# Kernel tuning notes

Hardware: AMD Instinct MI355X
Metric: run time of the kernel (lower is better)

Reference implementation:

```python
import jax, jax.numpy as jnp
import numpy as np

N = 100000   # nodes
E = 1600000  # edges
D = 128      # input feature dim
H = 64       # hidden dim
G = 64       # graphs in batch


def setup_inputs() -> dict:
    key = jax.random.key(0)
    ks = jax.random.split(key, 12)
    x = jax.random.normal(ks[0], (N, D), dtype=jnp.float32)
    ei = jax.random.randint(ks[1], (2, E), 0, N, dtype=jnp.int32)
    ew = jax.random.uniform(ks[2], (E,), dtype=jnp.float32)
    b = jnp.sort(jax.random.randint(ks[3], (N,), 0, G, dtype=jnp.int32))
    s = 0.05
    W1 = jax.random.normal(ks[4], (D, H), jnp.float32) * s
    b1 = jnp.zeros((H,), jnp.float32)
    W2 = jax.random.normal(ks[5], (H, H), jnp.float32) * s
    b2 = jnp.zeros((H,), jnp.float32)
    Wm1 = jax.random.normal(ks[6], (H, 32), jnp.float32) * s
    bm1 = jnp.zeros((32,), jnp.float32)
    Wm2 = jax.random.normal(ks[7], (32, 1), jnp.float32) * s
    bm2 = jnp.zeros((1,), jnp.float32)
    return {"x": x, "ei": ei, "ew": ew, "b": b,
            "W1": W1, "b1": b1, "W2": W2, "b2": b2,
            "Wm1": Wm1, "bm1": bm1, "Wm2": Wm2, "bm2": bm2}


def _gcn_norm(ei, ew, n):
    # PyG gcn_norm with add_self_loops=True (self-loop weight 1)
    loops = jnp.arange(n, dtype=ei.dtype)
    row = jnp.concatenate([ei[0], loops])
    col = jnp.concatenate([ei[1], loops])
    w = jnp.concatenate([ew, jnp.ones((n,), ew.dtype)])
    deg = jax.ops.segment_sum(w, col, num_segments=n)
    dinv = jnp.where(deg > 0, jax.lax.rsqrt(deg), 0.0)
    norm = dinv[row] * w * dinv[col]  # [E+N]
    return row, col, norm


def _gcn_conv(x, W, bias, row, col, norm, n):
    h = x @ W                                   # [N,H] small GEMM
    msg = h[row] * norm[:, None]                # gather over edges
    return jax.ops.segment_sum(msg, col, num_segments=n) + bias


def reference(x, ei, ew, b, W1, b1, W2, b2, Wm1, bm1, Wm2, bm2):
    n = x.shape[0]
    row, col, norm = _gcn_norm(ei, ew, n)
    h = jax.nn.relu(_gcn_conv(x, W1, b1, row, col, norm, n))
    h = jax.nn.relu(_gcn_conv(h, W2, b2, row, col, norm, n))
    # global_mean_pool over batch vector b
    sums = jax.ops.segment_sum(h, b, num_segments=G)
    cnt = jax.ops.segment_sum(jnp.ones((n,), h.dtype), b, num_segments=G)
    pooled = sums / jnp.maximum(cnt, 1.0)[:, None]  # [G,H]
    # MLP head: Linear(H,32) -> ReLU -> Linear(32,1)
    return jax.nn.relu(pooled @ Wm1 + bm1) @ Wm2 + bm2
```

## Files before the change

### kernel.cpp

```cpp
#include <hip/hip_runtime.h>
#include <hip/hip_bf16.h>
#include <hip/hip_fp16.h>


#define DIMH 64
#define BSH 7
#define BSZ 128
#define NBUCK_MAX 1024
#define EPB 4096
#define ESTRIDE 3072
#define CSTRIDE 4096

typedef _Float16 v8h __attribute__((ext_vector_type(8)));
typedef float v4f __attribute__((ext_vector_type(4)));

__global__ __launch_bounds__(512) void k_part(const int* __restrict__ row,
                                              const int* __restrict__ col,
                                              const float* __restrict__ ew,
                                              int* __restrict__ cursor,
                                              unsigned long long* __restrict__ part,
                                              int E, int nbuck) {
    __shared__ int h[NBUCK_MAX];
    __shared__ int h2[NBUCK_MAX];
    __shared__ int st[NBUCK_MAX];
    for (int i = threadIdx.x; i < nbuck; i += 512) { h[i] = 0; h2[i] = 0; }
    __syncthreads();
    int ebeg = blockIdx.x * EPB;
    int eend = min(ebeg + EPB, E);
    for (int e = ebeg + threadIdx.x; e < eend; e += 512)
        atomicAdd(&h[col[e] >> BSH], 1);
    __syncthreads();
    for (int i = threadIdx.x; i < nbuck; i += 512) {
        int c = h[i];
        st[i] = c ? i * ESTRIDE + atomicAdd(&cursor[i], c) : 0;
    }
    __syncthreads();
    for (int e = ebeg + threadIdx.x; e < eend; e += 512) {
        int c = col[e];
        int b = c >> BSH;
        int r = atomicAdd(&h2[b], 1);
        int slot = st[b] + r;
        if (slot < (b + 1) * ESTRIDE) {
            unsigned long long rec =
                ((unsigned long long)__float_as_uint(ew[e]) << 32) |
                ((unsigned long long)(unsigned)row[e] << 8) |
                (unsigned)(c & (BSZ - 1));
            part[slot] = rec;
        }
    }
}

__global__ __launch_bounds__(256) void k_sortB(const unsigned long long* __restrict__ part,
                                               const int* __restrict__ cursor,
                                               int2* __restrict__ csr,
                                               unsigned* __restrict__ rp,
                                               float* __restrict__ dinv, int N) {
    __shared__ int cnt[BSZ];
    __shared__ int scn[BSZ];
    __shared__ int cur[BSZ];
    __shared__ float dg[BSZ];
    int b = blockIdx.x;
    int nb0 = b << BSH;
    int nn = min(BSZ, N - nb0);
    int tid = threadIdx.x;
    if (tid < BSZ) { cnt[tid] = 0; dg[tid] = 1.0f; }
    __syncthreads();
    int ebeg = b * ESTRIDE;
    int eend = ebeg + min(cursor[b], ESTRIDE);
    for (int e = ebeg + tid; e < eend; e += 256)
        atomicAdd(&cnt[(int)(part[e] & (BSZ - 1))], 1);
    __syncthreads();
    int pc = 0;
    if (tid < BSZ) pc = min((cnt[tid] + 7) & ~7, 504);
    if (tid < BSZ) scn[tid] = pc;
    __syncthreads();
    for (int o = 1; o < BSZ; o <<= 1) {
        int t = 0;
        if (tid >= o && tid < BSZ) t = scn[tid - o];
        __syncthreads();
        if (tid >= o && tid < BSZ) scn[tid] += t;
        __syncthreads();
    }
    int Pb = b * CSTRIDE;
    int pofs = 0;
    if (tid < BSZ) {
        pofs = scn[tid] - pc;
        cur[tid] = pofs;
        if (tid < nn)
            rp[nb0 + tid] = ((unsigned)(pc >> 3) << 26) | (unsigned)(Pb + pofs);
    }
    __syncthreads();
    for (int e = ebeg + tid; e < eend; e += 256) {
        unsigned long long rec = part[e];
        int cl = (int)(rec & (BSZ - 1));
        float w = __uint_as_float((unsigned)(rec >> 32));
        int slot = atomicAdd(&cur[cl], 1);
        csr[Pb + slot] = make_int2((int)((rec >> 8) & 0xFFFFFF), __float_as_int(w));
        atomicAdd(&dg[cl], w);
    }
    __syncthreads();
    if (tid < nn) {
        int c = min(cnt[tid], pc);
        for (int k = c; k < pc; k++)
            csr[Pb + pofs + k] = make_int2(nb0 + tid, 0);
        dinv[nb0 + tid] = rsqrtf(dg[tid]);
    }
}

__global__ __launch_bounds__(256) void k_gemm_mfma(const float* __restrict__ X,
                                                   const float* __restrict__ W,
                                                   const float* __restrict__ dinv,
                                                   __half* __restrict__ Y, int n) {
    __shared__ _Float16 Wh[128 * 64];
    int tid = threadIdx.x;
    for (int i = tid * 4; i < 128 * 64; i += 256 * 4) {
        float4 w = *(const float4*)&W[i];
        Wh[i]     = (_Float16)w.x;
        Wh[i + 1] = (_Float16)w.y;
        Wh[i + 2] = (_Float16)w.z;
        Wh[i + 3] = (_Float16)w.w;
    }
    __syncthreads();

    int wv = tid >> 6;
    int lane = tid & 63;
    int m = lane & 15;
    int quad = lane >> 4;
    int tile = blockIdx.x * 4 + wv;
    int ntiles = (n + 15) >> 4;
    if (tile >= ntiles) return;

    v8h bf[4][4];
#pragma unroll
    for (int nt = 0; nt < 4; nt++)
#pragma unroll
        for (int s = 0; s < 4; s++)
#pragma unroll
            for (int j = 0; j < 8; j++)
                bf[nt][s][j] = Wh[(s * 32 + quad * 8 + j) * 64 + nt * 16 + m];

    v4f acc[4];
#pragma unroll
    for (int nt = 0; nt < 4; nt++) acc[nt] = (v4f){0.f, 0.f, 0.f, 0.f};

    int row = min(tile * 16 + m, n - 1);
    const float* xr = X + (size_t)row * 128;
#pragma unroll
    for (int s = 0; s < 4; s++) {
        float4 lo = *(const float4*)&xr[s * 32 + quad * 8];
        float4 hi = *(const float4*)&xr[s * 32 + quad * 8 + 4];
        v8h af;
        af[0] = (_Float16)lo.x; af[1] = (_Float16)lo.y;
        af[2] = (_Float16)lo.z; af[3] = (_Float16)lo.w;
        af[4] = (_Float16)hi.x; af[5] = (_Float16)hi.y;
        af[6] = (_Float16)hi.z; af[7] = (_Float16)hi.w;
#pragma unroll
        for (int nt = 0; nt < 4; nt++)
            acc[nt] = __builtin_amdgcn_mfma_f32_16x16x32_f16(af, bf[nt][s], acc[nt], 0, 0, 0);
    }

#pragma unroll
    for (int r = 0; r < 4; r++) {
        int node = tile * 16 + quad * 4 + r;
        if (node < n) {
            float di = dinv[node];
#pragma unroll
            for (int nt = 0; nt < 4; nt++)
                Y[(size_t)node * DIMH + nt * 16 + m] = __float2half(di * acc[nt][r]);
        }
    }
}

__global__ __launch_bounds__(256) void k_agg1f(const __half* __restrict__ Hin,
                                               const unsigned* __restrict__ rp,
                                               const int2* __restrict__ csr,
                                               const float* __restrict__ dinv,
                                               const float* __restrict__ bias,
                                               const float* __restrict__ W2,
                                               __half* __restrict__ T2, int n) {
    __shared__ float W2s[DIMH * DIMH];
    __shared__ unsigned hbuf[4][32];
    int tid = threadIdx.x;
    for (int i = tid * 4; i < DIMH * DIMH; i += 256 * 4)
        *(float4*)&W2s[i] = *(const float4*)&W2[i];
    __syncthreads();

    int lane = tid & 63;
    int wv = tid >> 6;
    int fp = lane & 31;
    bool hi = lane >= 32;
    const unsigned* HinU = (const unsigned*)Hin;
    int ngroups = (n + 3) >> 2;

    for (int grp = blockIdx.x; grp < ngroups; grp += gridDim.x) {
        int node = grp * 4 + wv;
        if (node >= n) continue;
        unsigned pk = rp[node];
        int p = (int)(pk & 0x3FFFFFFu);
        int iters = (int)(pk >> 26);
        float ax = 0.f, ay = 0.f;
        if (!hi) {
            unsigned su = HinU[(size_t)node * 32 + fp];
            float2 sf = __half22float2(*(__half2*)&su);
            ax = sf.x; ay = sf.y;
        }
        for (int it = 0; it < iters; it++, p += 8) {
            int4 m0 = *(const int4*)&csr[p];
            int4 m1 = *(const int4*)&csr[p + 2];
            int4 m2 = *(const int4*)&csr[p + 4];
            int4 m3 = *(const int4*)&csr[p + 6];
            int   s0 = hi ? m0.z : m0.x;
            float w0 = __int_as_float(hi ? m0.w : m0.y);
            int   s1 = hi ? m1.z : m1.x;
            float w1 = __int_as_float(hi ? m1.w : m1.y);
            int   s2 = hi ? m2.z : m2.x;
            float w2 = __int_as_float(hi ? m2.w : m2.y);
            int   s3 = hi ? m3.z : m3.x;
            float w3 = __int_as_float(hi ? m3.w : m3.y);
            unsigned u0 = HinU[(size_t)s0 * 32 + fp];
            unsigned u1 = HinU[(size_t)s1 * 32 + fp];
            unsigned u2 = HinU[(size_t)s2 * 32 + fp];
            unsigned u3 = HinU[(size_t)s3 * 32 + fp];
            float2 f0 = __half22float2(*(__half2*)&u0);
            float2 f1 = __half22float2(*(__half2*)&u1);
            float2 f2 = __half22float2(*(__half2*)&u2);
            float2 f3 = __half22float2(*(__half2*)&u3);
            ax += w0 * f0.x; ay += w0 * f0.y;
            ax += w1 * f1.x; ay += w1 * f1.y;
            ax += w2 * f2.x; ay += w2 * f2.y;
            ax += w3 * f3.x; ay += w3 * f3.y;
        }
        ax += __shfl_xor(ax, 32, 64);
        ay += __shfl_xor(ay, 32, 64);
        float di = dinv[node];
        if (!hi) {
            float vx = di * ax + bias[2 * fp];
            float vy = di * ay + bias[2 * fp + 1];
            vx = vx > 0.f ? vx : 0.f;
            vy = vy > 0.f ? vy : 0.f;
            __half2 hh = __floats2half2_rn(vx, vy);
            hbuf[wv][fp] = *(unsigned*)&hh;
        }
        float acc2 = 0.f;
        const unsigned* hb = hbuf[wv];
#pragma unroll
        for (int k8 = 0; k8 < 8; k8++) {
            uint4 hc = *(const uint4*)&hb[k8 * 4];
            float2 g0 = __half22float2(*(__half2*)&hc.x);
            float2 g1 = __half22float2(*(__half2*)&hc.y);
            float2 g2 = __half22float2(*(__half2*)&hc.z);
            float2 g3 = __half22float2(*(__half2*)&hc.w);
            const float* wc = &W2s[(k8 * 8) * DIMH + lane];
            acc2 += g0.x * wc[0 * DIMH] + g0.y * wc[1 * DIMH]
                  + g1.x * wc[2 * DIMH] + g1.y * wc[3 * DIMH]
                  + g2.x * wc[4 * DIMH] + g2.y * wc[5 * DIMH]
                  + g3.x * wc[6 * DIMH] + g3.y * wc[7 * DIMH];
        }
        T2[(size_t)node * DIMH + lane] = __float2half(di * acc2);
    }
}

__global__ __launch_bounds__(256) void k_aggN(const __half* __restrict__ Hin,
                                              const unsigned* __restrict__ rp,
                                              const int2* __restrict__ csr,
                                              const float* __restrict__ dinv,
                                              const float* __restrict__ bias,
                                              __half* __restrict__ Hout, int n) {
    int lane = threadIdx.x & 63;
    int wv = threadIdx.x >> 6;
    int node = blockIdx.x * 4 + wv;
    if (node >= n) return;
    unsigned pk = rp[node];
    int p = (int)(pk & 0x3FFFFFFu);
    int iters = (int)(pk >> 26);
    int fp = lane & 31;
    bool hi = lane >= 32;
    const unsigned* HinU = (const unsigned*)Hin;
    float ax = 0.f, ay = 0.f;
    if (!hi) {
        unsigned su = HinU[(size_t)node * 32 + fp];
        float2 sf = __half22float2(*(__half2*)&su);
        ax = sf.x; ay = sf.y;
    }
    for (int it = 0; it < iters; it++, p += 8) {
        int4 m0 = *(const int4*)&csr[p];
        int4 m1 = *(const int4*)&csr[p + 2];
        int4 m2 = *(const int4*)&csr[p + 4];
        int4 m3 = *(const int4*)&csr[p + 6];
        int   s0 = hi ? m0.z : m0.x;
        float w0 = __int_as_float(hi ? m0.w : m0.y);
        int   s1 = hi ? m1.z : m1.x;
        float w1 = __int_as_float(hi ? m1.w : m1.y);
        int   s2 = hi ? m2.z : m2.x;
        float w2 = __int_as_float(hi ? m2.w : m2.y);
        int   s3 = hi ? m3.z : m3.x;
        float w3 = __int_as_float(hi ? m3.w : m3.y);
        unsigned u0 = HinU[(size_t)s0 * 32 + fp];
        unsigned u1 = HinU[(size_t)s1 * 32 + fp];
        unsigned u2 = HinU[(size_t)s2 * 32 + fp];
        unsigned u3 = HinU[(size_t)s3 * 32 + fp];
        float2 f0 = __half22float2(*(__half2*)&u0);
        float2 f1 = __half22float2(*(__half2*)&u1);
        float2 f2 = __half22float2(*(__half2*)&u2);
        float2 f3 = __half22float2(*(__half2*)&u3);
        ax += w0 * f0.x; ay += w0 * f0.y;
        ax += w1 * f1.x; ay += w1 * f1.y;
        ax += w2 * f2.x; ay += w2 * f2.y;
        ax += w3 * f3.x; ay += w3 * f3.y;
    }
    ax += __shfl_xor(ax, 32, 64);
    ay += __shfl_xor(ay, 32, 64);
    if (!hi) {
        float di = dinv[node];
        float vx = di * ax + bias[2 * fp];
        float vy = di * ay + bias[2 * fp + 1];
        vx = vx > 0.f ? vx : 0.f;
        vy = vy > 0.f ? vy : 0.f;
        __half2 o = __floats2half2_rn(vx, vy);
        *(__half2*)&Hout[(size_t)node * DIMH + 2 * fp] = o;
    }
}

__global__ __launch_bounds__(256) void k_pool(const __half* __restrict__ Hin,
                                              const int* __restrict__ b,
                                              float* __restrict__ sums,
                                              float* __restrict__ cntG, int n) {
    const int CHUNK = 64;
    int lane = threadIdx.x & 63;
    int wave = threadIdx.x >> 6;
    int start = (blockIdx.x * 4 + wave) * CHUNK;
    if (start >= n) return;
    int end = min(start + CHUNK, n);
    float acc = 0.f;
    int g_cur = b[start];
    int cnt_local = 0;
    for (int i = start; i < end; i++) {
        int g = b[i];
        if (g != g_cur) {
            atomicAdd(&sums[g_cur * DIMH + lane], acc);
            if (lane == 0) atomicAdd(&cntG[g_cur], (float)cnt_local);
            acc = 0.f;
            cnt_local = 0;
            g_cur = g;
        }
        acc += __half2float(Hin[(size_t)i * DIMH + lane]);
        cnt_local++;
    }
    atomicAdd(&sums[g_cur * DIMH + lane], acc);
    if (lane == 0) atomicAdd(&cntG[g_cur], (float)cnt_local);
}

__global__ __launch_bounds__(64) void k_mlp(const float* __restrict__ sums,
                                            const float* __restrict__ cntG,
                                            const float* __restrict__ Wm1,
                                            const float* __restrict__ bm1,
                                            const float* __restrict__ Wm2,
                                            const float* __restrict__ bm2,
                                            float* __restrict__ out, int G) {
    int g = threadIdx.x;
    if (g >= G) return;
    float c = cntG[g];
    float inv = 1.f / (c > 1.f ? c : 1.f);
    float pooled[DIMH];
#pragma unroll
    for (int k = 0; k < DIMH; k++) pooled[k] = sums[g * DIMH + k] * inv;
    float o = 0.f;
    for (int j = 0; j < 32; j++) {
        float t = bm1[j];
#pragma unroll
        for (int k = 0; k < DIMH; k++) t += pooled[k] * Wm1[k * 32 + j];
        t = t > 0.f ? t : 0.f;
        o += t * Wm2[j];
    }
    out[g] = o + bm2[0];
}


extern "C" void kernel_launch(void* const* d_in, const int* in_sizes, int n_in,
                              void* d_out, int out_size, void* d_ws, size_t ws_size,
                              hipStream_t stream) {
    const float* x   = (const float*)d_in[0];
    const int*   ei  = (const int*)d_in[1];
    const float* ew  = (const float*)d_in[2];
    const int*   bvec= (const int*)d_in[3];
    const float* W1  = (const float*)d_in[4];
    const float* b1  = (const float*)d_in[5];
    const float* W2  = (const float*)d_in[6];
    const float* b2  = (const float*)d_in[7];
    const float* Wm1 = (const float*)d_in[8];
    const float* bm1 = (const float*)d_in[9];
    const float* Wm2 = (const float*)d_in[10];
    const float* bm2 = (const float*)d_in[11];
    float* out = (float*)d_out;

    const int E = in_sizes[2];
    const int N = in_sizes[3];
    const int G = out_size;
    const int* row = ei;
    const int* col = ei + E;
    const int nbuck = (N + BSZ - 1) >> BSH;

    char* p = (char*)d_ws;
    auto alloc = [&](size_t bytes) {
        void* r = (void*)p;
        p += (bytes + 255) & ~(size_t)255;
        return r;
    };

    unsigned long long* part = (unsigned long long*)alloc((size_t)nbuck * ESTRIDE * 8);
    int2*  csr    = (int2*)alloc((size_t)nbuck * CSTRIDE * 8);
    unsigned* rp  = (unsigned*)alloc((size_t)N * 4);
    float* dinv   = (float*)alloc((size_t)N * 4);
    __half* hA    = (__half*)alloc((size_t)N * DIMH * 2);
    __half* hB    = (__half*)alloc((size_t)N * DIMH * 2);
    int zeroInts  = nbuck + G * DIMH + G;
    int* cursor   = (int*)alloc((size_t)zeroInts * 4);
    float* sums   = (float*)(cursor + nbuck);
    float* cntG   = sums + G * DIMH;

    hipMemsetAsync(cursor, 0, (size_t)zeroInts * 4, stream);

    const int PB = (E + EPB - 1) / EPB;
    const int NT = (N + 15) / 16;

    k_part<<<PB, 512, 0, stream>>>(row, col, ew, cursor, part, E, nbuck);
    k_sortB<<<nbuck, 256, 0, stream>>>(part, cursor, csr, rp, dinv, N);

    k_gemm_mfma<<<(NT + 3) / 4, 256, 0, stream>>>(x, W1, dinv, hA, N);

    k_agg1f<<<4096, 256, 0, stream>>>(hA, rp, csr, dinv, b1, W2, hB, N);

    k_aggN<<<(N + 3) / 4, 256, 0, stream>>>(hB, rp, csr, dinv, b2, hA, N);

    k_pool<<<(N + 255) / 256, 256, 0, stream>>>(hA, bvec, sums, cntG, N);
    k_mlp<<<1, 64, 0, stream>>>(sums, cntG, Wm1, bm1, Wm2, bm2, out, G);
}
```

Baseline: 336.2 us.

## Split wave into four edge quarters with 8-byte gathers and MFMA layer-2 transform

The aggregation kernels now split each wave into four 16-lane groups, each gathering one 4-half (8-byte) feature slice per neighbor. Each iteration covers 16 edges instead of 8, so CSR padding moves to multiples of 16. The fused layer-1 kernel replaces its scalar LDS matvec with W2 in fp16 LDS and MFMA 16x16x32 instructions, keeping the B fragments in registers. This aims to raise the number of gathers in flight per wave and cut ALU work, at the cost of more padding edges, extra shuffle reductions and fp16 rounding of W2.

```diff
diff --git a/kernel.cpp b/kernel.cpp
--- a/kernel.cpp
+++ b/kernel.cpp
@@ -71,7 +71,7 @@
         atomicAdd(&cnt[(int)(part[e] & (BSZ - 1))], 1);
     __syncthreads();
     int pc = 0;
-    if (tid < BSZ) pc = min((cnt[tid] + 7) & ~7, 504);
+    if (tid < BSZ) pc = min((cnt[tid] + 15) & ~15, 496);
     if (tid < BSZ) scn[tid] = pc;
     __syncthreads();
     for (int o = 1; o < BSZ; o <<= 1) {
@@ -87,7 +87,7 @@
         pofs = scn[tid] - pc;
         cur[tid] = pofs;
         if (tid < nn)
-            rp[nb0 + tid] = ((unsigned)(pc >> 3) << 26) | (unsigned)(Pb + pofs);
+            rp[nb0 + tid] = ((unsigned)(pc >> 4) << 26) | (unsigned)(Pb + pofs);
     }
     __syncthreads();
     for (int e = ebeg + tid; e < eend; e += 256) {
@@ -178,85 +178,96 @@
                                                const float* __restrict__ bias,
                                                const float* __restrict__ W2,
                                                __half* __restrict__ T2, int n) {
-    __shared__ float W2s[DIMH * DIMH];
-    __shared__ unsigned hbuf[4][32];
+    __shared__ _Float16 W2h[DIMH * DIMH];
+    __shared__ __align__(16) _Float16 hbuf[4][DIMH];
     int tid = threadIdx.x;
-    for (int i = tid * 4; i < DIMH * DIMH; i += 256 * 4)
-        *(float4*)&W2s[i] = *(const float4*)&W2[i];
+    for (int i = tid * 4; i < DIMH * DIMH; i += 256 * 4) {
+        float4 w = *(const float4*)&W2[i];
+        W2h[i]     = (_Float16)w.x;
+        W2h[i + 1] = (_Float16)w.y;
+        W2h[i + 2] = (_Float16)w.z;
+        W2h[i + 3] = (_Float16)w.w;
+    }
     __syncthreads();
 
     int lane = tid & 63;
     int wv = tid >> 6;
-    int fp = lane & 31;
-    bool hi = lane >= 32;
-    const unsigned* HinU = (const unsigned*)Hin;
+    int q = lane >> 4;
+    int fp = lane & 15;
+
+    v8h bf[4][2];
+#pragma unroll
+    for (int nt = 0; nt < 4; nt++)
+#pragma unroll
+        for (int s = 0; s < 2; s++)
+#pragma unroll
+            for (int j = 0; j < 8; j++)
+                bf[nt][s][j] = W2h[(s * 32 + q * 8 + j) * DIMH + nt * 16 + fp];
+
+    const uint2* H2 = (const uint2*)Hin;
     int ngroups = (n + 3) >> 2;
-
     for (int grp = blockIdx.x; grp < ngroups; grp += gridDim.x) {
         int node = grp * 4 + wv;
         if (node >= n) continue;
         unsigned pk = rp[node];
         int p = (int)(pk & 0x3FFFFFFu);
         int iters = (int)(pk >> 26);
-        float ax = 0.f, ay = 0.f;
-        if (!hi) {
-            unsigned su = HinU[(size_t)node * 32 + fp];
-            float2 sf = __half22float2(*(__half2*)&su);
-            ax = sf.x; ay = sf.y;
-        }
-        for (int it = 0; it < iters; it++, p += 8) {
-            int4 m0 = *(const int4*)&csr[p];
-            int4 m1 = *(const int4*)&csr[p + 2];
-            int4 m2 = *(const int4*)&csr[p + 4];
-            int4 m3 = *(const int4*)&csr[p + 6];
-            int   s0 = hi ? m0.z : m0.x;
-            float w0 = __int_as_float(hi ? m0.w : m0.y);
-            int   s1 = hi ? m1.z : m1.x;
-            float w1 = __int_as_float(hi ? m1.w : m1.y);
-            int   s2 = hi ? m2.z : m2.x;
-            float w2 = __int_as_float(hi ? m2.w : m2.y);
-            int   s3 = hi ? m3.z : m3.x;
-            float w3 = __int_as_float(hi ? m3.w : m3.y);
-            unsigned u0 = HinU[(size_t)s0 * 32 + fp];
-            unsigned u1 = HinU[(size_t)s1 * 32 + fp];
-            unsigned u2 = HinU[(size_t)s2 * 32 + fp];
-            unsigned u3 = HinU[(size_t)s3 * 32 + fp];
-            float2 f0 = __half22float2(*(__half2*)&u0);
-            float2 f1 = __half22float2(*(__half2*)&u1);
-            float2 f2 = __half22float2(*(__half2*)&u2);
-            float2 f3 = __half22float2(*(__half2*)&u3);
-            ax += w0 * f0.x; ay += w0 * f0.y;
-            ax += w1 * f1.x; ay += w1 * f1.y;
-            ax += w2 * f2.x; ay += w2 * f2.y;
-            ax += w3 * f3.x; ay += w3 * f3.y;
-        }
-        ax += __shfl_xor(ax, 32, 64);
-        ay += __shfl_xor(ay, 32, 64);
+        float a0 = 0.f, a1 = 0.f, a2 = 0.f, a3 = 0.f;
+        if (q == 0) {
+            uint2 su = H2[(size_t)node * 16 + fp];
+            float2 f0 = __half22float2(*(__half2*)&su.x);
+            float2 f1 = __half22float2(*(__half2*)&su.y);
+            a0 = f0.x; a1 = f0.y; a2 = f1.x; a3 = f1.y;
+        }
+        for (int it = 0; it < iters; it++, p += 16) {
+            int4 mA = *(const int4*)&csr[p + 2 * q];
+            int4 mB = *(const int4*)&csr[p + 8 + 2 * q];
+            uint2 u0 = H2[(size_t)mA.x * 16 + fp];
+            uint2 u1 = H2[(size_t)mA.z * 16 + fp];
+            uint2 u2 = H2[(size_t)mB.x * 16 + fp];
+            uint2 u3 = H2[(size_t)mB.z * 16 + fp];
+            float w0 = __int_as_float(mA.y), w1 = __int_as_float(mA.w);
+            float w2 = __int_as_float(mB.y), w3 = __int_as_float(mB.w);
+            float2 f;
+            f = __half22float2(*(__half2*)&u0.x); a0 += w0 * f.x; a1 += w0 * f.y;
+            f = __half22float2(*(__half2*)&u0.y); a2 += w0 * f.x; a3 += w0 * f.y;
+            f = __half22float2(*(__half2*)&u1.x); a0 += w1 * f.x; a1 += w1 * f.y;
+            f = __half22float2(*(__half2*)&u1.y); a2 += w1 * f.x; a3 += w1 * f.y;
+            f = __half22float2(*(__half2*)&u2.x); a0 += w2 * f.x; a1 += w2 * f.y;
+            f = __half22float2(*(__half2*)&u2.y); a2 += w2 * f.x; a3 += w2 * f.y;
+            f = __half22float2(*(__half2*)&u3.x); a0 += w3 * f.x; a1 += w3 * f.y;
+            f = __half22float2(*(__half2*)&u3.y); a2 += w3 * f.x; a3 += w3 * f.y;
+        }
+        a0 += __shfl_xor(a0, 16, 64); a0 += __shfl_xor(a0, 32, 64);
+        a1 += __shfl_xor(a1, 16, 64); a1 += __shfl_xor(a1, 32, 64);
+        a2 += __shfl_xor(a2, 16, 64); a2 += __shfl_xor(a2, 32, 64);
+        a3 += __shfl_xor(a3, 16, 64); a3 += __shfl_xor(a3, 32, 64);
         float di = dinv[node];
-        if (!hi) {
-            float vx = di * ax + bias[2 * fp];
-            float vy = di * ay + bias[2 * fp + 1];
-            vx = vx > 0.f ? vx : 0.f;
-            vy = vy > 0.f ? vy : 0.f;
-            __half2 hh = __floats2half2_rn(vx, vy);
-            hbuf[wv][fp] = *(unsigned*)&hh;
-        }
-        float acc2 = 0.f;
-        const unsigned* hb = hbuf[wv];
-#pragma unroll
-        for (int k8 = 0; k8 < 8; k8++) {
-            uint4 hc = *(const uint4*)&hb[k8 * 4];
-            float2 g0 = __half22float2(*(__half2*)&hc.x);
-            float2 g1 = __half22float2(*(__half2*)&hc.y);
-            float2 g2 = __half22float2(*(__half2*)&hc.z);
-            float2 g3 = __half22float2(*(__half2*)&hc.w);
-            const float* wc = &W2s[(k8 * 8) * DIMH + lane];
-            acc2 += g0.x * wc[0 * DIMH] + g0.y * wc[1 * DIMH]
-                  + g1.x * wc[2 * DIMH] + g1.y * wc[3 * DIMH]
-                  + g2.x * wc[4 * DIMH] + g2.y * wc[5 * DIMH]
-                  + g3.x * wc[6 * DIMH] + g3.y * wc[7 * DIMH];
-        }
-        T2[(size_t)node * DIMH + lane] = __float2half(di * acc2);
+        if (q == 0) {
+            float4 bs = *(const float4*)&bias[fp * 4];
+            float v0 = fmaxf(di * a0 + bs.x, 0.f);
+            float v1 = fmaxf(di * a1 + bs.y, 0.f);
+            float v2 = fmaxf(di * a2 + bs.z, 0.f);
+            float v3 = fmaxf(di * a3 + bs.w, 0.f);
+            __half2 h0 = __floats2half2_rn(v0, v1);
+            __half2 h1 = __floats2half2_rn(v2, v3);
+            uint2 o;
+            o.x = *(unsigned*)&h0;
+            o.y = *(unsigned*)&h1;
+            *(uint2*)&hbuf[wv][fp * 4] = o;
+        }
+        v4f c0 = (v4f){0.f, 0.f, 0.f, 0.f};
+        v4f c1 = c0, c2 = c0, c3 = c0;
+#pragma unroll
+        for (int s = 0; s < 2; s++) {
+            v8h af = *(const v8h*)&hbuf[wv][s * 32 + q * 8];
+            c0 = __builtin_amdgcn_mfma_f32_16x16x32_f16(af, bf[0][s], c0, 0, 0, 0);
+            c1 = __builtin_amdgcn_mfma_f32_16x16x32_f16(af, bf[1][s], c1, 0, 0, 0);
+            c2 = __builtin_amdgcn_mfma_f32_16x16x32_f16(af, bf[2][s], c2, 0, 0, 0);
+            c3 = __builtin_amdgcn_mfma_f32_16x16x32_f16(af, bf[3][s], c3, 0, 0, 0);
+        }
+        float y = q == 0 ? c0[0] : q == 1 ? c1[0] : q == 2 ? c2[0] : c3[0];
+        T2[(size_t)node * DIMH + lane] = __float2half(di * y);
     }
 }
 
@@ -273,51 +284,52 @@
     unsigned pk = rp[node];
     int p = (int)(pk & 0x3FFFFFFu);
     int iters = (int)(pk >> 26);
-    int fp = lane & 31;
-    bool hi = lane >= 32;
-    const unsigned* HinU = (const unsigned*)Hin;
-    float ax = 0.f, ay = 0.f;
-    if (!hi) {
-        unsigned su = HinU[(size_t)node * 32 + fp];
-        float2 sf = __half22float2(*(__half2*)&su);
-        ax = sf.x; ay = sf.y;
-    }
-    for (int it = 0; it < iters; it++, p += 8) {
-        int4 m0 = *(const int4*)&csr[p];
-        int4 m1 = *(const int4*)&csr[p + 2];
-        int4 m2 = *(const int4*)&csr[p + 4];
-        int4 m3 = *(const int4*)&csr[p + 6];
-        int   s0 = hi ? m0.z : m0.x;
-        float w0 = __int_as_float(hi ? m0.w : m0.y);
-        int   s1 = hi ? m1.z : m1.x;
-        float w1 = __int_as_float(hi ? m1.w : m1.y);
-        int   s2 = hi ? m2.z : m2.x;
-        float w2 = __int_as_float(hi ? m2.w : m2.y);
-        int   s3 = hi ? m3.z : m3.x;
-        float w3 = __int_as_float(hi ? m3.w : m3.y);
-        unsigned u0 = HinU[(size_t)s0 * 32 + fp];
-        unsigned u1 = HinU[(size_t)s1 * 32 + fp];
-        unsigned u2 = HinU[(size_t)s2 * 32 + fp];
-        unsigned u3 = HinU[(size_t)s3 * 32 + fp];
-        float2 f0 = __half22float2(*(__half2*)&u0);
-        float2 f1 = __half22float2(*(__half2*)&u1);
-        float2 f2 = __half22float2(*(__half2*)&u2);
-        float2 f3 = __half22float2(*(__half2*)&u3);
-        ax += w0 * f0.x; ay += w0 * f0.y;
-        ax += w1 * f1.x; ay += w1 * f1.y;
-        ax += w2 * f2.x; ay += w2 * f2.y;
-        ax += w3 * f3.x; ay += w3 * f3.y;
-    }
-    ax += __shfl_xor(ax, 32, 64);
-    ay += __shfl_xor(ay, 32, 64);
-    if (!hi) {
+    int q = lane >> 4;
+    int fp = lane & 15;
+    const uint2* H2 = (const uint2*)Hin;
+    float a0 = 0.f, a1 = 0.f, a2 = 0.f, a3 = 0.f;
+    if (q == 0) {
+        uint2 su = H2[(size_t)node * 16 + fp];
+        float2 f0 = __half22float2(*(__half2*)&su.x);
+        float2 f1 = __half22float2(*(__half2*)&su.y);
+        a0 = f0.x; a1 = f0.y; a2 = f1.x; a3 = f1.y;
+    }
+    for (int it = 0; it < iters; it++, p += 16) {
+        int4 mA = *(const int4*)&csr[p + 2 * q];
+        int4 mB = *(const int4*)&csr[p + 8 + 2 * q];
+        uint2 u0 = H2[(size_t)mA.x * 16 + fp];
+        uint2 u1 = H2[(size_t)mA.z * 16 + fp];
+        uint2 u2 = H2[(size_t)mB.x * 16 + fp];
+        uint2 u3 = H2[(size_t)mB.z * 16 + fp];
+        float w0 = __int_as_float(mA.y), w1 = __int_as_float(mA.w);
+        float w2 = __int_as_float(mB.y), w3 = __int_as_float(mB.w);
+        float2 f;
+        f = __half22float2(*(__half2*)&u0.x); a0 += w0 * f.x; a1 += w0 * f.y;
+        f = __half22float2(*(__half2*)&u0.y); a2 += w0 * f.x; a3 += w0 * f.y;
+        f = __half22float2(*(__half2*)&u1.x); a0 += w1 * f.x; a1 += w1 * f.y;
+        f = __half22float2(*(__half2*)&u1.y); a2 += w1 * f.x; a3 += w1 * f.y;
+        f = __half22float2(*(__half2*)&u2.x); a0 += w2 * f.x; a1 += w2 * f.y;
+        f = __half22float2(*(__half2*)&u2.y); a2 += w2 * f.x; a3 += w2 * f.y;
+        f = __half22float2(*(__half2*)&u3.x); a0 += w3 * f.x; a1 += w3 * f.y;
+        f = __half22float2(*(__half2*)&u3.y); a2 += w3 * f.x; a3 += w3 * f.y;
+    }
+    a0 += __shfl_xor(a0, 16, 64); a0 += __shfl_xor(a0, 32, 64);
+    a1 += __shfl_xor(a1, 16, 64); a1 += __shfl_xor(a1, 32, 64);
+    a2 += __shfl_xor(a2, 16, 64); a2 += __shfl_xor(a2, 32, 64);
+    a3 += __shfl_xor(a3, 16, 64); a3 += __shfl_xor(a3, 32, 64);
+    if (q == 0) {
         float di = dinv[node];
-        float vx = di * ax + bias[2 * fp];
-        float vy = di * ay + bias[2 * fp + 1];
-        vx = vx > 0.f ? vx : 0.f;
-        vy = vy > 0.f ? vy : 0.f;
-        __half2 o = __floats2half2_rn(vx, vy);
-        *(__half2*)&Hout[(size_t)node * DIMH + 2 * fp] = o;
+        float4 bs = *(const float4*)&bias[fp * 4];
+        float v0 = fmaxf(di * a0 + bs.x, 0.f);
+        float v1 = fmaxf(di * a1 + bs.y, 0.f);
+        float v2 = fmaxf(di * a2 + bs.z, 0.f);
+        float v3 = fmaxf(di * a3 + bs.w, 0.f);
+        __half2 h0 = __floats2half2_rn(v0, v1);
+        __half2 h1 = __floats2half2_rn(v2, v3);
+        uint2 o;
+        o.x = *(unsigned*)&h0;
+        o.y = *(unsigned*)&h1;
+        *(uint2*)&Hout[(size_t)node * DIMH + fp * 4] = o;
     }
 }
 
```

Result: no change. 333.7 us (-0.7%).
